# Optimization experiments

Hardware: AMD Instinct MI355X
Metric: run time of the kernel (lower is better)

The kernel has to match this reference:

```python
import jax, jax.numpy as jnp
import numpy as np

NUM_HEADS = 16


def setup_inputs() -> dict:
    key = jax.random.key(0)
    k1, k2, k3 = jax.random.split(key, 3)
    B, N, C = 8, 1024, 1024
    x = jax.random.normal(k1, (B, N, C), dtype=jnp.float32)
    w_qkv = jax.random.normal(k2, (3 * C, C), dtype=jnp.float32) * (C ** -0.5)
    w_proj = jax.random.normal(k3, (C, C), dtype=jnp.float32) * (C ** -0.5)
    b_proj = jnp.zeros((C,), dtype=jnp.float32)
    return {"x": x, "w_qkv": w_qkv, "w_proj": w_proj, "b_proj": b_proj}


def reference(x, w_qkv, w_proj, b_proj):
    B, N, C = x.shape
    H = NUM_HEADS
    d = C // H
    scale = d ** -0.5
    # qkv projection: (B, N, 3C) -> (3, B, H, N, d)
    qkv = jnp.einsum('bnc,oc->bno', x, w_qkv)
    qkv = qkv.reshape(B, N, 3, H, d).transpose(2, 0, 3, 1, 4)
    q, k, v = qkv[0], qkv[1], qkv[2]
    # spatial attention
    attn = jnp.einsum('bhnd,bhmd->bhnm', q, k) * scale
    attn = jax.nn.softmax(attn, axis=-1)
    out = jnp.einsum('bhnm,bhmd->bhnd', attn, v)
    out = out.transpose(0, 2, 1, 3).reshape(B, N, C)
    # output projection
    return jnp.einsum('bnc,oc->bno', out, w_proj) + b_proj
```

## Files before the change

### kernel.cpp

```cpp
#include <hip/hip_runtime.h>
#include <hip/hip_bf16.h>

typedef unsigned short u16;
typedef unsigned int u32;
typedef __bf16 bf16x8 __attribute__((ext_vector_type(8)));
typedef float f32x4 __attribute__((ext_vector_type(4)));

__device__ __forceinline__ u16 f2b(float f) {
    __bf16 h = (__bf16)f;
    return __builtin_bit_cast(u16, h);
}
__device__ __forceinline__ u32 f2b2(float lo, float hi) {
    return (u32)f2b(lo) | ((u32)f2b(hi) << 16);
}
__device__ __forceinline__ f32x4 mfma16(bf16x8 a, bf16x8 b, f32x4 c) {
    return __builtin_amdgcn_mfma_f32_16x16x32_bf16(a, b, c, 0, 0, 0);
}
__device__ __forceinline__ void async16(const u16* gsrc, u16* ldst) {
    __builtin_amdgcn_global_load_lds(
        (const __attribute__((address_space(1))) void*)gsrc,
        (__attribute__((address_space(3))) void*)ldst, 16, 0, 0);
}

__global__ __launch_bounds__(256) void cvt_all(const float* __restrict__ x,
                                               const float* __restrict__ wq,
                                               const float* __restrict__ wp,
                                               u16* __restrict__ xb,
                                               u16* __restrict__ wqb,
                                               u16* __restrict__ wpb) {
    int i = (blockIdx.x * 256 + threadIdx.x) * 4;
    const float* src; u16* dst; int off; float scl;
    if (i < 8388608)       { src = x;  dst = xb;  off = i;            scl = 1.f; }
    else if (i < 9437184)  { src = wq; dst = wqb; off = i - 8388608;  scl = 0.18033688f; }
    else if (i < 11534336) { src = wq; dst = wqb; off = i - 8388608;  scl = 1.f; }
    else                   { src = wp; dst = wpb; off = i - 11534336; scl = 1.f; }
    float4 f = *(const float4*)(src + off);
    ushort4 o;
    o.x = f2b(f.x * scl); o.y = f2b(f.y * scl);
    o.z = f2b(f.z * scl); o.w = f2b(f.w * scl);
    *(ushort4*)(dst + off) = o;
}

template <bool F32OUT>
__device__ __forceinline__ void gemm_core(const u16* __restrict__ A,
                                          const u16* __restrict__ B,
                                          void* __restrict__ Cptr,
                                          const float* __restrict__ bias,
                                          int N, int K, int bm, int bn,
                                          u16* As, u16* Bs) {
    const int tid  = threadIdx.x;
    const int lane = tid & 63, wid = tid >> 6;
    const int quad = lane >> 4, l16 = lane & 15;
    const int wm = (wid >> 1) * 64, wn = (wid & 1) * 64;
    const int swr = l16 & 7;

    const int srow8  = lane >> 3;
    const int schunk = ((lane & 7) ^ srow8) << 3;

    const u16* Abase = A + (size_t)(bm * 128) * K;
    const u16* Bbase = B + (size_t)(bn * 128) * K;

    f32x4 acc[4][4] = {};

    for (int k0 = 0; k0 < K; k0 += 64) {
        __syncthreads();
#pragma unroll
        for (int j = 0; j < 4; ++j) {
            int rg = wid * 32 + j * 8;
            async16(Abase + (size_t)(rg + srow8) * K + k0 + schunk, &As[rg * 64]);
            async16(Bbase + (size_t)(rg + srow8) * K + k0 + schunk, &Bs[rg * 64]);
        }
        __syncthreads();
#pragma unroll
        for (int s = 0; s < 2; ++s) {
            bf16x8 af[4], bfr[4];
#pragma unroll
            for (int mt = 0; mt < 4; mt++) {
                int r = wm + mt * 16 + l16;
                af[mt] = *(const bf16x8*)&As[r * 64 + (((s * 4 + quad) ^ swr) << 3)];
            }
#pragma unroll
            for (int nt = 0; nt < 4; nt++) {
                int r = wn + nt * 16 + l16;
                bfr[nt] = *(const bf16x8*)&Bs[r * 64 + (((s * 4 + quad) ^ swr) << 3)];
            }
#pragma unroll
            for (int mt = 0; mt < 4; mt++)
#pragma unroll
                for (int nt = 0; nt < 4; nt++)
                    acc[mt][nt] = mfma16(af[mt], bfr[nt], acc[mt][nt]);
        }
    }
#pragma unroll
    for (int mt = 0; mt < 4; mt++) {
#pragma unroll
        for (int nt = 0; nt < 4; nt++) {
            int row = bm * 128 + wm + mt * 16 + quad * 4;
            int col = bn * 128 + wn + nt * 16 + l16;
            float bv = F32OUT ? bias[col] : 0.f;
#pragma unroll
            for (int r = 0; r < 4; r++) {
                if (F32OUT)
                    ((float*)Cptr)[(size_t)(row + r) * N + col] = acc[mt][nt][r] + bv;
                else
                    ((u16*)Cptr)[(size_t)(row + r) * N + col] = f2b(acc[mt][nt][r]);
            }
        }
    }
}

__global__ __launch_bounds__(256) void gemm_qkvt(const u16* __restrict__ xb,
                                                 const u16* __restrict__ wqkvb,
                                                 u16* __restrict__ qkb,
                                                 u16* __restrict__ vTb) {
    __shared__ u16 As[128 * 64];
    __shared__ u16 Bs[128 * 64];
    int id = blockIdx.x;
    if (id < 1024) {
        gemm_core<false>(xb, wqkvb, qkb, nullptr, 2048, 1024, id >> 4, id & 15, As, Bs);
    } else {
        int t = id - 1024;
        gemm_core<false>(wqkvb + (size_t)2048 * 1024, xb, vTb, nullptr,
                         8192, 1024, t >> 6, t & 63, As, Bs);
    }
}

__global__ __launch_bounds__(256) void gemm_proj(const u16* __restrict__ A,
                                                 const u16* __restrict__ B,
                                                 void* __restrict__ C,
                                                 const float* __restrict__ bias) {
    __shared__ u16 As[128 * 64];
    __shared__ u16 Bs[128 * 64];
    gemm_core<true>(A, B, C, bias, 1024, 1024, blockIdx.y, blockIdx.x, As, Bs);
}

__global__ __launch_bounds__(256, 4) void attn_kernel(const u16* __restrict__ qk,
                                                      const u16* __restrict__ vT,
                                                      u16* __restrict__ outb) {
    __shared__ u16 Ks[2][64 * 64];
    __shared__ u16 Vt[2][64 * 64];
    __shared__ u16 Ps[4 * 16 * 64];
    const int tid = threadIdx.x, lane = tid & 63, wid = tid >> 6;
    const int quad = lane >> 4, l16 = lane & 15;
    const int qt = blockIdx.x;
    const int bh = blockIdx.y;
    const int b = bh >> 4, h = bh & 15;
    const size_t base = (size_t)b * 1024;
    const int hoff = h * 64;

    const int sr_ = lane >> 3;
    const int sc_ = ((lane & 7) ^ sr_) * 8;
    const int sw = l16 & 7;

    const u16* qptr = qk + (base + qt * 64 + wid * 16 + l16) * 2048 + hoff + quad * 8;
    bf16x8 bq0 = *(const bf16x8*)qptr;
    bf16x8 bq1 = *(const bf16x8*)(qptr + 32);

    auto stageK = [&](int kt, int bs) {
#pragma unroll
        for (int j = 0; j < 2; ++j) {
            int rg = wid * 16 + j * 8;
            async16(qk + (base + kt * 64 + rg + sr_) * 2048 + 1024 + hoff + sc_,
                    &Ks[bs][rg * 64]);
        }
    };
    auto stageV = [&](int kt, int bs) {
#pragma unroll
        for (int j = 0; j < 2; ++j) {
            int rg = wid * 16 + j * 8;
            async16(vT + (size_t)(hoff + rg + sr_) * 8192 + base + kt * 64 + sc_,
                    &Vt[bs][rg * 64]);
        }
    };
    stageK(0, 0);

    f32x4 Oacc[4] = {};
    f32x4 lacc = {};
    bf16x8 vone;
#pragma unroll
    for (int i = 0; i < 8; ++i) vone[i] = (__bf16)1.0f;
    u16* Pw = &Ps[wid * (16 * 64)];
    bf16x8 ap0, ap1;

    for (int u = 0; u < 16; ++u) {
        const int cur = u & 1;
        __builtin_amdgcn_s_barrier();
        __builtin_amdgcn_sched_barrier(0);
        if (u < 15) stageK(u + 1, cur ^ 1);
        stageV(u, cur);
        if (u < 15) asm volatile("s_waitcnt vmcnt(4)" ::: "memory");
        else        asm volatile("s_waitcnt vmcnt(2)" ::: "memory");
        __builtin_amdgcn_s_barrier();
        __builtin_amdgcn_sched_barrier(0);

        f32x4 sacc[4] = {};
#pragma unroll
        for (int nt = 0; nt < 4; nt++) {
            int row = nt * 16 + l16;
            bf16x8 ak0 = *(const bf16x8*)&Ks[cur][row * 64 + ((quad ^ sw) << 3)];
            bf16x8 ak1 = *(const bf16x8*)&Ks[cur][row * 64 + (((4 + quad) ^ sw) << 3)];
            sacc[nt] = mfma16(ak0, bq0, sacc[nt]);
            sacc[nt] = mfma16(ak1, bq1, sacc[nt]);
        }

        if (u) {
            lacc = mfma16(ap0, vone, lacc);
#pragma unroll
            for (int nv = 0; nv < 4; nv++) {
                int row = nv * 16 + l16;
                bf16x8 bv = *(const bf16x8*)&Vt[cur ^ 1][row * 64 + ((quad ^ sw) << 3)];
                Oacc[nv] = mfma16(ap0, bv, Oacc[nv]);
            }
        }
#pragma unroll
        for (int nt = 0; nt < 2; nt++) {
            float p0 = exp2f(sacc[nt][0]);
            float p1 = exp2f(sacc[nt][1]);
            float p2 = exp2f(sacc[nt][2]);
            float p3 = exp2f(sacc[nt][3]);
            uint2 pk; pk.x = f2b2(p0, p1); pk.y = f2b2(p2, p3);
            *(uint2*)&Pw[l16 * 64 + (((nt * 2 + (quad >> 1)) ^ sw) << 3) + ((quad & 1) << 2)] = pk;
        }
        if (u) {
            lacc = mfma16(ap1, vone, lacc);
#pragma unroll
            for (int nv = 0; nv < 4; nv++) {
                int row = nv * 16 + l16;
                bf16x8 bv = *(const bf16x8*)&Vt[cur ^ 1][row * 64 + (((4 + quad) ^ sw) << 3)];
                Oacc[nv] = mfma16(ap1, bv, Oacc[nv]);
            }
        }
#pragma unroll
        for (int nt = 2; nt < 4; nt++) {
            float p0 = exp2f(sacc[nt][0]);
            float p1 = exp2f(sacc[nt][1]);
            float p2 = exp2f(sacc[nt][2]);
            float p3 = exp2f(sacc[nt][3]);
            uint2 pk; pk.x = f2b2(p0, p1); pk.y = f2b2(p2, p3);
            *(uint2*)&Pw[l16 * 64 + (((nt * 2 + (quad >> 1)) ^ sw) << 3) + ((quad & 1) << 2)] = pk;
        }

        asm volatile("s_waitcnt lgkmcnt(0)" ::: "memory");
        __builtin_amdgcn_wave_barrier();
        __builtin_amdgcn_sched_barrier(0);
        ap0 = *(const bf16x8*)&Pw[l16 * 64 + ((quad ^ sw) << 3)];
        ap1 = *(const bf16x8*)&Pw[l16 * 64 + (((4 + quad) ^ sw) << 3)];
    }

    asm volatile("s_waitcnt vmcnt(0)" ::: "memory");
    __builtin_amdgcn_s_barrier();
    __builtin_amdgcn_sched_barrier(0);
    lacc = mfma16(ap0, vone, lacc);
#pragma unroll
    for (int nv = 0; nv < 4; nv++) {
        int row = nv * 16 + l16;
        bf16x8 bv = *(const bf16x8*)&Vt[1][row * 64 + ((quad ^ sw) << 3)];
        Oacc[nv] = mfma16(ap0, bv, Oacc[nv]);
    }
    lacc = mfma16(ap1, vone, lacc);
#pragma unroll
    for (int nv = 0; nv < 4; nv++) {
        int row = nv * 16 + l16;
        bf16x8 bv = *(const bf16x8*)&Vt[1][row * 64 + (((4 + quad) ^ sw) << 3)];
        Oacc[nv] = mfma16(ap1, bv, Oacc[nv]);
    }

    float inv[4];
#pragma unroll
    for (int r = 0; r < 4; r++) inv[r] = 1.f / lacc[r];

#pragma unroll
    for (int nv = 0; nv < 4; nv++)
#pragma unroll
        for (int r = 0; r < 4; r++) {
            int row = qt * 64 + wid * 16 + quad * 4 + r;
            int col = hoff + nv * 16 + l16;
            outb[(base + row) * 1024 + col] = f2b(Oacc[nv][r] * inv[r]);
        }
}

extern "C" void kernel_launch(void* const* d_in, const int* in_sizes, int n_in,
                              void* d_out, int out_size, void* d_ws, size_t ws_size,
                              hipStream_t stream) {
    const float* x      = (const float*)d_in[0];
    const float* w_qkv  = (const float*)d_in[1];
    const float* w_proj = (const float*)d_in[2];
    const float* b_proj = (const float*)d_in[3];

    char* ws = (char*)d_ws;
    u16* xb     = (u16*)(ws);
    u16* wqkvb  = (u16*)(ws + 16777216);
    u16* wprojb = (u16*)(ws + 23068672);
    u16* qkb    = (u16*)(ws + 25165824);
    u16* vTb    = (u16*)(ws + 58720256);
    u16* attnb  = (u16*)(ws + 75497472);

    cvt_all<<<12288, 256, 0, stream>>>(x, w_qkv, w_proj, xb, wqkvb, wprojb);
    gemm_qkvt<<<1536, 256, 0, stream>>>(xb, wqkvb, qkb, vTb);
    attn_kernel<<<dim3(16, 128), 256, 0, stream>>>(qkb, vTb, attnb);
    gemm_proj<<<dim3(8, 64), 256, 0, stream>>>(attnb, wprojb, d_out, b_proj);
}
```

Measured before the change: 245.3 us.

## Process two 64-row query tiles per attention block to reuse staged K/V

Each attention block now handles 128 query rows as two 64-row halves sharing the same staged K and V tiles in LDS, halving the grid in x. This is meant to halve the global-to-LDS traffic for K/V per query row and amortize barriers. In exchange, register pressure roughly doubles for accumulators, the grid is halved (1024 blocks), and the two halves share one P scratch buffer per wave, serialized by waitcnt and wave barriers.

```diff
diff --git a/kernel.cpp b/kernel.cpp
--- a/kernel.cpp
+++ b/kernel.cpp
@@ -152,9 +152,12 @@
     const int sc_ = ((lane & 7) ^ sr_) * 8;
     const int sw = l16 & 7;
 
-    const u16* qptr = qk + (base + qt * 64 + wid * 16 + l16) * 2048 + hoff + quad * 8;
-    bf16x8 bq0 = *(const bf16x8*)qptr;
-    bf16x8 bq1 = *(const bf16x8*)(qptr + 32);
+    const u16* qptrA = qk + (base + qt * 128 + wid * 16 + l16) * 2048 + hoff + quad * 8;
+    const u16* qptrB = qptrA + (size_t)64 * 2048;
+    bf16x8 bqA0 = *(const bf16x8*)qptrA;
+    bf16x8 bqA1 = *(const bf16x8*)(qptrA + 32);
+    bf16x8 bqB0 = *(const bf16x8*)qptrB;
+    bf16x8 bqB1 = *(const bf16x8*)(qptrB + 32);
 
     auto stageK = [&](int kt, int bs) {
 #pragma unroll
@@ -174,13 +177,67 @@
     };
     stageK(0, 0);
 
-    f32x4 Oacc[4] = {};
-    f32x4 lacc = {};
+    f32x4 OaccA[4] = {}, OaccB[4] = {};
+    f32x4 laccA = {}, laccB = {};
     bf16x8 vone;
 #pragma unroll
     for (int i = 0; i < 8; ++i) vone[i] = (__bf16)1.0f;
     u16* Pw = &Ps[wid * (16 * 64)];
-    bf16x8 ap0, ap1;
+    bf16x8 apA0, apA1, apB0, apB1;
+
+    auto do_half = [&](f32x4 (&Oacc)[4], f32x4& lacc, bf16x8& ap0, bf16x8& ap1,
+                       bf16x8 bq0, bf16x8 bq1, int cur, bool dopv) {
+        f32x4 sacc[4] = {};
+#pragma unroll
+        for (int nt = 0; nt < 4; nt++) {
+            int row = nt * 16 + l16;
+            bf16x8 ak0 = *(const bf16x8*)&Ks[cur][row * 64 + ((quad ^ sw) << 3)];
+            bf16x8 ak1 = *(const bf16x8*)&Ks[cur][row * 64 + (((4 + quad) ^ sw) << 3)];
+            sacc[nt] = mfma16(ak0, bq0, sacc[nt]);
+            sacc[nt] = mfma16(ak1, bq1, sacc[nt]);
+        }
+        if (dopv) {
+            lacc = mfma16(ap0, vone, lacc);
+#pragma unroll
+            for (int nv = 0; nv < 4; nv++) {
+                int row = nv * 16 + l16;
+                bf16x8 bv = *(const bf16x8*)&Vt[cur ^ 1][row * 64 + ((quad ^ sw) << 3)];
+                Oacc[nv] = mfma16(ap0, bv, Oacc[nv]);
+            }
+        }
+#pragma unroll
+        for (int nt = 0; nt < 2; nt++) {
+            float p0 = exp2f(sacc[nt][0]);
+            float p1 = exp2f(sacc[nt][1]);
+            float p2 = exp2f(sacc[nt][2]);
+            float p3 = exp2f(sacc[nt][3]);
+            uint2 pk; pk.x = f2b2(p0, p1); pk.y = f2b2(p2, p3);
+            *(uint2*)&Pw[l16 * 64 + (((nt * 2 + (quad >> 1)) ^ sw) << 3) + ((quad & 1) << 2)] = pk;
+        }
+        if (dopv) {
+            lacc = mfma16(ap1, vone, lacc);
+#pragma unroll
+            for (int nv = 0; nv < 4; nv++) {
+                int row = nv * 16 + l16;
+                bf16x8 bv = *(const bf16x8*)&Vt[cur ^ 1][row * 64 + (((4 + quad) ^ sw) << 3)];
+                Oacc[nv] = mfma16(ap1, bv, Oacc[nv]);
+            }
+        }
+#pragma unroll
+        for (int nt = 2; nt < 4; nt++) {
+            float p0 = exp2f(sacc[nt][0]);
+            float p1 = exp2f(sacc[nt][1]);
+            float p2 = exp2f(sacc[nt][2]);
+            float p3 = exp2f(sacc[nt][3]);
+            uint2 pk; pk.x = f2b2(p0, p1); pk.y = f2b2(p2, p3);
+            *(uint2*)&Pw[l16 * 64 + (((nt * 2 + (quad >> 1)) ^ sw) << 3) + ((quad & 1) << 2)] = pk;
+        }
+        asm volatile("s_waitcnt lgkmcnt(0)" ::: "memory");
+        __builtin_amdgcn_wave_barrier();
+        __builtin_amdgcn_sched_barrier(0);
+        ap0 = *(const bf16x8*)&Pw[l16 * 64 + ((quad ^ sw) << 3)];
+        ap1 = *(const bf16x8*)&Pw[l16 * 64 + (((4 + quad) ^ sw) << 3)];
+    };
 
     for (int u = 0; u < 16; ++u) {
         const int cur = u & 1;
@@ -193,89 +250,44 @@
         __builtin_amdgcn_s_barrier();
         __builtin_amdgcn_sched_barrier(0);
 
-        f32x4 sacc[4] = {};
-#pragma unroll
-        for (int nt = 0; nt < 4; nt++) {
-            int row = nt * 16 + l16;
-            bf16x8 ak0 = *(const bf16x8*)&Ks[cur][row * 64 + ((quad ^ sw) << 3)];
-            bf16x8 ak1 = *(const bf16x8*)&Ks[cur][row * 64 + (((4 + quad) ^ sw) << 3)];
-            sacc[nt] = mfma16(ak0, bq0, sacc[nt]);
-            sacc[nt] = mfma16(ak1, bq1, sacc[nt]);
-        }
-
-        if (u) {
-            lacc = mfma16(ap0, vone, lacc);
-#pragma unroll
-            for (int nv = 0; nv < 4; nv++) {
-                int row = nv * 16 + l16;
-                bf16x8 bv = *(const bf16x8*)&Vt[cur ^ 1][row * 64 + ((quad ^ sw) << 3)];
-                Oacc[nv] = mfma16(ap0, bv, Oacc[nv]);
-            }
-        }
-#pragma unroll
-        for (int nt = 0; nt < 2; nt++) {
-            float p0 = exp2f(sacc[nt][0]);
-            float p1 = exp2f(sacc[nt][1]);
-            float p2 = exp2f(sacc[nt][2]);
-            float p3 = exp2f(sacc[nt][3]);
-            uint2 pk; pk.x = f2b2(p0, p1); pk.y = f2b2(p2, p3);
-            *(uint2*)&Pw[l16 * 64 + (((nt * 2 + (quad >> 1)) ^ sw) << 3) + ((quad & 1) << 2)] = pk;
-        }
-        if (u) {
-            lacc = mfma16(ap1, vone, lacc);
-#pragma unroll
-            for (int nv = 0; nv < 4; nv++) {
-                int row = nv * 16 + l16;
-                bf16x8 bv = *(const bf16x8*)&Vt[cur ^ 1][row * 64 + (((4 + quad) ^ sw) << 3)];
-                Oacc[nv] = mfma16(ap1, bv, Oacc[nv]);
-            }
-        }
-#pragma unroll
-        for (int nt = 2; nt < 4; nt++) {
-            float p0 = exp2f(sacc[nt][0]);
-            float p1 = exp2f(sacc[nt][1]);
-            float p2 = exp2f(sacc[nt][2]);
-            float p3 = exp2f(sacc[nt][3]);
-            uint2 pk; pk.x = f2b2(p0, p1); pk.y = f2b2(p2, p3);
-            *(uint2*)&Pw[l16 * 64 + (((nt * 2 + (quad >> 1)) ^ sw) << 3) + ((quad & 1) << 2)] = pk;
-        }
-
-        asm volatile("s_waitcnt lgkmcnt(0)" ::: "memory");
-        __builtin_amdgcn_wave_barrier();
-        __builtin_amdgcn_sched_barrier(0);
-        ap0 = *(const bf16x8*)&Pw[l16 * 64 + ((quad ^ sw) << 3)];
-        ap1 = *(const bf16x8*)&Pw[l16 * 64 + (((4 + quad) ^ sw) << 3)];
+        do_half(OaccA, laccA, apA0, apA1, bqA0, bqA1, cur, u != 0);
+        do_half(OaccB, laccB, apB0, apB1, bqB0, bqB1, cur, u != 0);
     }
 
     asm volatile("s_waitcnt vmcnt(0)" ::: "memory");
     __builtin_amdgcn_s_barrier();
     __builtin_amdgcn_sched_barrier(0);
-    lacc = mfma16(ap0, vone, lacc);
-#pragma unroll
-    for (int nv = 0; nv < 4; nv++) {
-        int row = nv * 16 + l16;
-        bf16x8 bv = *(const bf16x8*)&Vt[1][row * 64 + ((quad ^ sw) << 3)];
-        Oacc[nv] = mfma16(ap0, bv, Oacc[nv]);
-    }
-    lacc = mfma16(ap1, vone, lacc);
-#pragma unroll
-    for (int nv = 0; nv < 4; nv++) {
-        int row = nv * 16 + l16;
-        bf16x8 bv = *(const bf16x8*)&Vt[1][row * 64 + (((4 + quad) ^ sw) << 3)];
-        Oacc[nv] = mfma16(ap1, bv, Oacc[nv]);
-    }
-
-    float inv[4];
-#pragma unroll
-    for (int r = 0; r < 4; r++) inv[r] = 1.f / lacc[r];
+    auto finish_half = [&](f32x4 (&Oacc)[4], f32x4& lacc, bf16x8 ap0, bf16x8 ap1) {
+        lacc = mfma16(ap0, vone, lacc);
+#pragma unroll
+        for (int nv = 0; nv < 4; nv++) {
+            int row = nv * 16 + l16;
+            bf16x8 bv = *(const bf16x8*)&Vt[1][row * 64 + ((quad ^ sw) << 3)];
+            Oacc[nv] = mfma16(ap0, bv, Oacc[nv]);
+        }
+        lacc = mfma16(ap1, vone, lacc);
+#pragma unroll
+        for (int nv = 0; nv < 4; nv++) {
+            int row = nv * 16 + l16;
+            bf16x8 bv = *(const bf16x8*)&Vt[1][row * 64 + (((4 + quad) ^ sw) << 3)];
+            Oacc[nv] = mfma16(ap1, bv, Oacc[nv]);
+        }
+    };
+    finish_half(OaccA, laccA, apA0, apA1);
+    finish_half(OaccB, laccB, apB0, apB1);
+
+    float invA[4], invB[4];
+#pragma unroll
+    for (int r = 0; r < 4; r++) { invA[r] = 1.f / laccA[r]; invB[r] = 1.f / laccB[r]; }
 
 #pragma unroll
     for (int nv = 0; nv < 4; nv++)
 #pragma unroll
         for (int r = 0; r < 4; r++) {
-            int row = qt * 64 + wid * 16 + quad * 4 + r;
-            int col = hoff + nv * 16 + l16;
-            outb[(base + row) * 1024 + col] = f2b(Oacc[nv][r] * inv[r]);
+            int rowA = qt * 128 + wid * 16 + quad * 4 + r;
+            int col  = hoff + nv * 16 + l16;
+            outb[(base + rowA) * 1024 + col]      = f2b(OaccA[nv][r] * invA[r]);
+            outb[(base + rowA + 64) * 1024 + col] = f2b(OaccB[nv][r] * invB[r]);
         }
 }
 
@@ -297,6 +309,6 @@
 
     cvt_all<<<12288, 256, 0, stream>>>(x, w_qkv, w_proj, xb, wqkvb, wprojb);
     gemm_qkvt<<<1536, 256, 0, stream>>>(xb, wqkvb, qkb, vTb);
-    attn_kernel<<<dim3(16, 128), 256, 0, stream>>>(qkb, vTb, attnb);
+    attn_kernel<<<dim3(8, 128), 256, 0, stream>>>(qkb, vTb, attnb);
     gemm_proj<<<dim3(8, 64), 256, 0, stream>>>(attnb, wprojb, d_out, b_proj);
 }
```

Result: no change. 249.2 us (+1.6%).

## Load K/V fragments directly from global memory instead of staging through LDS

Applied to the files above, without the earlier changes.

The attention kernel drops the double-buffered LDS staging of K and V tiles, along with the block-level barriers that guarded it. Each wave now loads its MFMA operand fragments for K and V directly from global memory into registers each iteration. This removes barrier synchronisation and LDS capacity use, which may permit higher occupancy. In exchange, every wave redundantly fetches the same K/V data, global-load latency is no longer hidden by asynchronous prefetch, and register pressure increases.

```diff
diff --git a/kernel.cpp b/kernel.cpp
--- a/kernel.cpp
+++ b/kernel.cpp
@@ -137,8 +137,6 @@
 __global__ __launch_bounds__(256, 4) void attn_kernel(const u16* __restrict__ qk,
                                                       const u16* __restrict__ vT,
                                                       u16* __restrict__ outb) {
-    __shared__ u16 Ks[2][64 * 64];
-    __shared__ u16 Vt[2][64 * 64];
     __shared__ u16 Ps[4 * 16 * 64];
     const int tid = threadIdx.x, lane = tid & 63, wid = tid >> 6;
     const int quad = lane >> 4, l16 = lane & 15;
@@ -147,32 +145,14 @@
     const int b = bh >> 4, h = bh & 15;
     const size_t base = (size_t)b * 1024;
     const int hoff = h * 64;
-
-    const int sr_ = lane >> 3;
-    const int sc_ = ((lane & 7) ^ sr_) * 8;
     const int sw = l16 & 7;
 
     const u16* qptr = qk + (base + qt * 64 + wid * 16 + l16) * 2048 + hoff + quad * 8;
     bf16x8 bq0 = *(const bf16x8*)qptr;
     bf16x8 bq1 = *(const bf16x8*)(qptr + 32);
 
-    auto stageK = [&](int kt, int bs) {
-#pragma unroll
-        for (int j = 0; j < 2; ++j) {
-            int rg = wid * 16 + j * 8;
-            async16(qk + (base + kt * 64 + rg + sr_) * 2048 + 1024 + hoff + sc_,
-                    &Ks[bs][rg * 64]);
-        }
-    };
-    auto stageV = [&](int kt, int bs) {
-#pragma unroll
-        for (int j = 0; j < 2; ++j) {
-            int rg = wid * 16 + j * 8;
-            async16(vT + (size_t)(hoff + rg + sr_) * 8192 + base + kt * 64 + sc_,
-                    &Vt[bs][rg * 64]);
-        }
-    };
-    stageK(0, 0);
+    const u16* kfrag = qk + (base + l16) * 2048 + 1024 + hoff + quad * 8;
+    const u16* vfrag = vT + ((size_t)(hoff + l16)) * 8192 + base + quad * 8;
 
     f32x4 Oacc[4] = {};
     f32x4 lacc = {};
@@ -183,33 +163,26 @@
     bf16x8 ap0, ap1;
 
     for (int u = 0; u < 16; ++u) {
-        const int cur = u & 1;
-        __builtin_amdgcn_s_barrier();
-        __builtin_amdgcn_sched_barrier(0);
-        if (u < 15) stageK(u + 1, cur ^ 1);
-        stageV(u, cur);
-        if (u < 15) asm volatile("s_waitcnt vmcnt(4)" ::: "memory");
-        else        asm volatile("s_waitcnt vmcnt(2)" ::: "memory");
-        __builtin_amdgcn_s_barrier();
-        __builtin_amdgcn_sched_barrier(0);
-
+        bf16x8 kk0[4], kk1[4];
+#pragma unroll
+        for (int nt = 0; nt < 4; nt++) {
+            const u16* kp = kfrag + (size_t)(u * 64 + nt * 16) * 2048;
+            kk0[nt] = *(const bf16x8*)kp;
+            kk1[nt] = *(const bf16x8*)(kp + 32);
+        }
         f32x4 sacc[4] = {};
 #pragma unroll
         for (int nt = 0; nt < 4; nt++) {
-            int row = nt * 16 + l16;
-            bf16x8 ak0 = *(const bf16x8*)&Ks[cur][row * 64 + ((quad ^ sw) << 3)];
-            bf16x8 ak1 = *(const bf16x8*)&Ks[cur][row * 64 + (((4 + quad) ^ sw) << 3)];
-            sacc[nt] = mfma16(ak0, bq0, sacc[nt]);
-            sacc[nt] = mfma16(ak1, bq1, sacc[nt]);
-        }
-
+            sacc[nt] = mfma16(kk0[nt], bq0, sacc[nt]);
+            sacc[nt] = mfma16(kk1[nt], bq1, sacc[nt]);
+        }
+        bf16x8 vv0[4], vv1[4];
         if (u) {
-            lacc = mfma16(ap0, vone, lacc);
 #pragma unroll
             for (int nv = 0; nv < 4; nv++) {
-                int row = nv * 16 + l16;
-                bf16x8 bv = *(const bf16x8*)&Vt[cur ^ 1][row * 64 + ((quad ^ sw) << 3)];
-                Oacc[nv] = mfma16(ap0, bv, Oacc[nv]);
+                const u16* vp = vfrag + (size_t)(nv * 16) * 8192 + (u - 1) * 64;
+                vv0[nv] = *(const bf16x8*)vp;
+                vv1[nv] = *(const bf16x8*)(vp + 32);
             }
         }
 #pragma unroll
@@ -222,13 +195,10 @@
             *(uint2*)&Pw[l16 * 64 + (((nt * 2 + (quad >> 1)) ^ sw) << 3) + ((quad & 1) << 2)] = pk;
         }
         if (u) {
-            lacc = mfma16(ap1, vone, lacc);
-#pragma unroll
-            for (int nv = 0; nv < 4; nv++) {
-                int row = nv * 16 + l16;
-                bf16x8 bv = *(const bf16x8*)&Vt[cur ^ 1][row * 64 + (((4 + quad) ^ sw) << 3)];
-                Oacc[nv] = mfma16(ap1, bv, Oacc[nv]);
-            }
+            lacc = mfma16(ap0, vone, lacc);
+#pragma unroll
+            for (int nv = 0; nv < 4; nv++)
+                Oacc[nv] = mfma16(ap0, vv0[nv], Oacc[nv]);
         }
 #pragma unroll
         for (int nt = 2; nt < 4; nt++) {
@@ -239,7 +209,12 @@
             uint2 pk; pk.x = f2b2(p0, p1); pk.y = f2b2(p2, p3);
             *(uint2*)&Pw[l16 * 64 + (((nt * 2 + (quad >> 1)) ^ sw) << 3) + ((quad & 1) << 2)] = pk;
         }
-
+        if (u) {
+            lacc = mfma16(ap1, vone, lacc);
+#pragma unroll
+            for (int nv = 0; nv < 4; nv++)
+                Oacc[nv] = mfma16(ap1, vv1[nv], Oacc[nv]);
+        }
         asm volatile("s_waitcnt lgkmcnt(0)" ::: "memory");
         __builtin_amdgcn_wave_barrier();
         __builtin_amdgcn_sched_barrier(0);
@@ -247,22 +222,22 @@
         ap1 = *(const bf16x8*)&Pw[l16 * 64 + (((4 + quad) ^ sw) << 3)];
     }
 
-    asm volatile("s_waitcnt vmcnt(0)" ::: "memory");
-    __builtin_amdgcn_s_barrier();
-    __builtin_amdgcn_sched_barrier(0);
-    lacc = mfma16(ap0, vone, lacc);
-#pragma unroll
-    for (int nv = 0; nv < 4; nv++) {
-        int row = nv * 16 + l16;
-        bf16x8 bv = *(const bf16x8*)&Vt[1][row * 64 + ((quad ^ sw) << 3)];
-        Oacc[nv] = mfma16(ap0, bv, Oacc[nv]);
-    }
-    lacc = mfma16(ap1, vone, lacc);
-#pragma unroll
-    for (int nv = 0; nv < 4; nv++) {
-        int row = nv * 16 + l16;
-        bf16x8 bv = *(const bf16x8*)&Vt[1][row * 64 + (((4 + quad) ^ sw) << 3)];
-        Oacc[nv] = mfma16(ap1, bv, Oacc[nv]);
+    {
+        bf16x8 vv0[4], vv1[4];
+#pragma unroll
+        for (int nv = 0; nv < 4; nv++) {
+            const u16* vp = vfrag + (size_t)(nv * 16) * 8192 + 15 * 64;
+            vv0[nv] = *(const bf16x8*)vp;
+            vv1[nv] = *(const bf16x8*)(vp + 32);
+        }
+        lacc = mfma16(ap0, vone, lacc);
+#pragma unroll
+        for (int nv = 0; nv < 4; nv++)
+            Oacc[nv] = mfma16(ap0, vv0[nv], Oacc[nv]);
+        lacc = mfma16(ap1, vone, lacc);
+#pragma unroll
+        for (int nv = 0; nv < 4; nv++)
+            Oacc[nv] = mfma16(ap1, vv1[nv], Oacc[nv]);
     }
 
     float inv[4];
```

Result: slower. 461.8 us (+88.2%).

## Double-buffer GEMM LDS tiles with a K-step of 32 and one barrier

Applied to the files above, without the earlier changes.

Restructures the shared GEMM core used by the QKV and output-projection kernels into a two-stage pipeline. Each K-step shrinks from 64 to 32, the LDS tiles are double-buffered, and the async global-to-LDS load of the next tile is issued before computing the current one. This replaces the two barriers per step with one. The goal is to hide global load latency behind the MFMA work. In exchange there are twice as many loop iterations and a new XOR swizzle for the 64-byte rows, which may change LDS bank-conflict behaviour.

```diff
diff --git a/kernel.cpp b/kernel.cpp
--- a/kernel.cpp
+++ b/kernel.cpp
@@ -52,44 +52,52 @@
     const int lane = tid & 63, wid = tid >> 6;
     const int quad = lane >> 4, l16 = lane & 15;
     const int wm = (wid >> 1) * 64, wn = (wid & 1) * 64;
-    const int swr = l16 & 7;
-
-    const int srow8  = lane >> 3;
-    const int schunk = ((lane & 7) ^ srow8) << 3;
+    const int swr = (l16 >> 1) & 3;
+
+    const int lr  = lane >> 2;
+    const int sch = ((lane & 3) ^ ((lr >> 1) & 3)) << 3;
 
     const u16* Abase = A + (size_t)(bm * 128) * K;
     const u16* Bbase = B + (size_t)(bn * 128) * K;
 
+    auto stage = [&](int k0, int buf) {
+        u16* as = As + buf * 4096;
+        u16* bs = Bs + buf * 4096;
+#pragma unroll
+        for (int j = 0; j < 2; ++j) {
+            int rg = wid * 32 + j * 16;
+            async16(Abase + (size_t)(rg + lr) * K + k0 + sch, &as[rg * 32]);
+            async16(Bbase + (size_t)(rg + lr) * K + k0 + sch, &bs[rg * 32]);
+        }
+    };
+
     f32x4 acc[4][4] = {};
-
-    for (int k0 = 0; k0 < K; k0 += 64) {
+    const int NT = K >> 5;
+    stage(0, 0);
+
+    for (int t = 0; t < NT; ++t) {
+        const int cur = t & 1;
         __syncthreads();
-#pragma unroll
-        for (int j = 0; j < 4; ++j) {
-            int rg = wid * 32 + j * 8;
-            async16(Abase + (size_t)(rg + srow8) * K + k0 + schunk, &As[rg * 64]);
-            async16(Bbase + (size_t)(rg + srow8) * K + k0 + schunk, &Bs[rg * 64]);
-        }
-        __syncthreads();
-#pragma unroll
-        for (int s = 0; s < 2; ++s) {
-            bf16x8 af[4], bfr[4];
-#pragma unroll
-            for (int mt = 0; mt < 4; mt++) {
-                int r = wm + mt * 16 + l16;
-                af[mt] = *(const bf16x8*)&As[r * 64 + (((s * 4 + quad) ^ swr) << 3)];
-            }
-#pragma unroll
-            for (int nt = 0; nt < 4; nt++) {
-                int r = wn + nt * 16 + l16;
-                bfr[nt] = *(const bf16x8*)&Bs[r * 64 + (((s * 4 + quad) ^ swr) << 3)];
-            }
-#pragma unroll
-            for (int mt = 0; mt < 4; mt++)
-#pragma unroll
-                for (int nt = 0; nt < 4; nt++)
-                    acc[mt][nt] = mfma16(af[mt], bfr[nt], acc[mt][nt]);
-        }
+        if (t + 1 < NT) stage((t + 1) << 5, cur ^ 1);
+
+        const u16* as = As + cur * 4096;
+        const u16* bs = Bs + cur * 4096;
+        bf16x8 af[4], bfr[4];
+#pragma unroll
+        for (int mt = 0; mt < 4; mt++) {
+            int r = wm + mt * 16 + l16;
+            af[mt] = *(const bf16x8*)&as[r * 32 + ((quad ^ swr) << 3)];
+        }
+#pragma unroll
+        for (int nt = 0; nt < 4; nt++) {
+            int r = wn + nt * 16 + l16;
+            bfr[nt] = *(const bf16x8*)&bs[r * 32 + ((quad ^ swr) << 3)];
+        }
+#pragma unroll
+        for (int mt = 0; mt < 4; mt++)
+#pragma unroll
+            for (int nt = 0; nt < 4; nt++)
+                acc[mt][nt] = mfma16(af[mt], bfr[nt], acc[mt][nt]);
     }
 #pragma unroll
     for (int mt = 0; mt < 4; mt++) {
@@ -113,8 +121,8 @@
                                                  const u16* __restrict__ wqkvb,
                                                  u16* __restrict__ qkb,
                                                  u16* __restrict__ vTb) {
-    __shared__ u16 As[128 * 64];
-    __shared__ u16 Bs[128 * 64];
+    __shared__ u16 As[2 * 128 * 32];
+    __shared__ u16 Bs[2 * 128 * 32];
     int id = blockIdx.x;
     if (id < 1024) {
         gemm_core<false>(xb, wqkvb, qkb, nullptr, 2048, 1024, id >> 4, id & 15, As, Bs);
@@ -129,8 +137,8 @@
                                                  const u16* __restrict__ B,
                                                  void* __restrict__ C,
                                                  const float* __restrict__ bias) {
-    __shared__ u16 As[128 * 64];
-    __shared__ u16 Bs[128 * 64];
+    __shared__ u16 As[2 * 128 * 32];
+    __shared__ u16 Bs[2 * 128 * 32];
     gemm_core<true>(A, B, C, bias, 1024, 1024, blockIdx.y, blockIdx.x, As, Bs);
 }
 
```

After: 262.6 us. 1.07x slower.
